# Kernel optimization log

Measured on AMD Instinct MI355X. Metric: run time of the kernel, lower is better.

Reference implementation:

```python
import jax, jax.numpy as jnp
import numpy as np

B, Q, D, H, HD, LP, M = 16, 1, 2048, 16, 128, 2048, 8192
EPS = 1e-5

def _ln(x, w, b):
    mu = jnp.mean(x, axis=-1, keepdims=True)
    var = jnp.mean((x - mu) ** 2, axis=-1, keepdims=True)
    return (x - mu) * jax.lax.rsqrt(var + EPS) * w + b

def setup_inputs() -> dict:
    key = jax.random.key(0)
    ks = jax.random.split(key, 8)
    std = 0.02
    return {
        "input": jax.random.normal(ks[0], (B, Q, D), jnp.float32),
        "past_key": jax.random.normal(ks[1], (B, LP, H, HD), jnp.float32),
        "past_value": jax.random.normal(ks[2], (B, LP, H, HD), jnp.float32),
        "ln0_w": jnp.ones((D,), jnp.float32),
        "ln0_b": jnp.zeros((D,), jnp.float32),
        "ln1_w": jnp.ones((D,), jnp.float32),
        "ln1_b": jnp.zeros((D,), jnp.float32),
        "wqkv": jax.random.normal(ks[3], (3 * D, D), jnp.float32) * std,
        "wo": jax.random.normal(ks[4], (D, D), jnp.float32) * std,
        "fc0_w": jax.random.normal(ks[5], (M, D), jnp.float32) * std,
        "fc0_b": jnp.zeros((M,), jnp.float32),
        "fc1_w": jax.random.normal(ks[6], (D, M), jnp.float32) * std,
        "fc1_b": jnp.zeros((D,), jnp.float32),
    }

def reference(input, past_key, past_value, ln0_w, ln0_b, ln1_w, ln1_b,
              wqkv, wo, fc0_w, fc0_b, fc1_w, fc1_b):
    # norm0 + fused QKV projection (no bias)
    x = _ln(input, ln0_w, ln0_b)                       # [B,Q,D]
    qkv = (x @ wqkv.T).reshape(B, Q, 3, H, HD)
    q, k, v = qkv[:, :, 0], qkv[:, :, 1], qkv[:, :, 2]  # each [B,Q,H,HD]
    # append to KV cache
    k = jnp.concatenate([past_key, k], axis=1)          # [B,LP+Q,H,HD]
    v = jnp.concatenate([past_value, v], axis=1)
    # decode attention; q_len == 1 so no causal mask is applied (matches source)
    scores = jnp.einsum('nqhd,nkhd->nhqk', q, k) / (HD ** 0.5)
    attn = jax.nn.softmax(scores.astype(jnp.float32), axis=-1).astype(scores.dtype)
    attn_out = jnp.einsum('nhql,nlhd->nqhd', attn, v).reshape(B, Q, D)
    attn_out = attn_out @ wo.T
    h = input + attn_out
    # MLP2 with exact (erf) GELU as in torch F.gelu
    y = _ln(h, ln1_w, ln1_b)
    y = jax.nn.gelu(y @ fc0_w.T + fc0_b, approximate=False) @ fc1_w.T + fc1_b
    return h + y
```

## Files before the change

kernel.cpp:

```cpp
#include <hip/hip_runtime.h>
#include <math.h>

typedef __attribute__((ext_vector_type(4))) float f32x4;
typedef __attribute__((ext_vector_type(4))) _Float16 f16x4;

#define B_  16
#define D_  2048
#define H_  16
#define HD_ 128
#define LP_ 2048
#define M_  8192
#define QKV_R (3 * D_)
#define SCALE 0.08838834764831845f
#define NSPLIT 32
#define KPS 64
#define TROWS 4
#define NT (KPS / TROWS)

__device__ inline float wave_sum(float v) {
  for (int m = 32; m > 0; m >>= 1) v += __shfl_xor(v, m);
  return v;
}

__device__ inline void gl_lds16(const float* g, float* l) {
  __builtin_amdgcn_global_load_lds(
      (const __attribute__((address_space(1))) void*)g,
      (__attribute__((address_space(3))) void*)l, 16, 0, 2 );
}

__global__ void ln_kernel(const float* __restrict__ x, const float* __restrict__ w,
                          const float* __restrict__ bb, float* __restrict__ o) {
  __shared__ float sred[4];
  int b = blockIdx.x, t = threadIdx.x;
  const float* xr = x + (size_t)b * D_;
  f32x4 v0 = *(const f32x4*)(xr + t * 8);
  f32x4 v1 = *(const f32x4*)(xr + t * 8 + 4);
  float s = (v0[0] + v0[1] + v0[2] + v0[3]) + (v1[0] + v1[1] + v1[2] + v1[3]);
  s = wave_sum(s);
  if ((t & 63) == 0) sred[t >> 6] = s;
  __syncthreads();
  float mu = (sred[0] + sred[1] + sred[2] + sred[3]) * (1.0f / D_);
  __syncthreads();
  float sq = 0.f;
  for (int i = 0; i < 4; i++) {
    float d0 = v0[i] - mu; sq += d0 * d0;
    float d1 = v1[i] - mu; sq += d1 * d1;
  }
  sq = wave_sum(sq);
  if ((t & 63) == 0) sred[t >> 6] = sq;
  __syncthreads();
  float var = (sred[0] + sred[1] + sred[2] + sred[3]) * (1.0f / D_);
  float rs = rsqrtf(var + 1e-5f);
  f32x4 w0 = *(const f32x4*)(w + t * 8), w1 = *(const f32x4*)(w + t * 8 + 4);
  f32x4 c0 = *(const f32x4*)(bb + t * 8), c1 = *(const f32x4*)(bb + t * 8 + 4);
  f32x4 o0, o1;
  for (int i = 0; i < 4; i++) {
    o0[i] = (v0[i] - mu) * rs * w0[i] + c0[i];
    o1[i] = (v1[i] - mu) * rs * w1[i] + c1[i];
  }
  *(f32x4*)(o + (size_t)b * D_ + t * 8) = o0;
  *(f32x4*)(o + (size_t)b * D_ + t * 8 + 4) = o1;
}

__global__ void gemv_k(const float* __restrict__ W, const float* __restrict__ X,
                       float* __restrict__ part, int R, int K, int kc) {
  int wave = threadIdx.x >> 6, lane = threadIdx.x & 63;
  int j0 = (blockIdx.x * 4 + wave) * 16;
  int k0 = blockIdx.y * kc;
  int col = lane & 15;
  int kg  = (lane >> 4) << 2;
  const float* wp = W + (size_t)(j0 + col) * K + k0 + kg;
  const float* xp = X + (size_t)col * K + k0 + kg;
  f32x4 acc = {0.f, 0.f, 0.f, 0.f};
  #pragma unroll 4
  for (int kk = 0; kk < kc; kk += 16) {
    f32x4 av = *(const f32x4*)xp; xp += 16;
    f32x4 bv = __builtin_nontemporal_load((const f32x4*)wp); wp += 16;
    f16x4 ah, bh;
    for (int i = 0; i < 4; i++) { ah[i] = (_Float16)av[i]; bh[i] = (_Float16)bv[i]; }
    acc = __builtin_amdgcn_mfma_f32_16x16x16f16(ah, bh, acc, 0, 0, 0);
  }
  *(f32x4*)(part + ((size_t)blockIdx.y * R + j0 + col) * 16 + kg) = acc;
}

__global__ void reduce_plain(const float* __restrict__ part, float* __restrict__ out,
                             int R, int S) {
  int i = blockIdx.x * 256 + threadIdx.x;
  int j = i >> 4, b = i & 15;
  float s = 0.f;
  for (int k = 0; k < S; k++) s += part[(size_t)k * R * 16 + i];
  out[(size_t)b * R + j] = s;
}
__global__ void reduce_resid(const float* __restrict__ part, const float* __restrict__ resid,
                             float* __restrict__ out, int R, int S) {
  int i = blockIdx.x * 256 + threadIdx.x;
  int j = i >> 4, b = i & 15;
  float s = 0.f;
  for (int k = 0; k < S; k++) s += part[(size_t)k * R * 16 + i];
  out[(size_t)b * R + j] = resid[(size_t)b * R + j] + s;
}
__global__ void reduce_bias_gelu(const float* __restrict__ part, const float* __restrict__ bias,
                                 float* __restrict__ out, int R, int S) {
  int i = blockIdx.x * 256 + threadIdx.x;
  int j = i >> 4, b = i & 15;
  float s = 0.f;
  for (int k = 0; k < S; k++) s += part[(size_t)k * R * 16 + i];
  float u = s + bias[j];
  out[(size_t)b * R + j] = 0.5f * u * (1.0f + erff(u * 0.70710678118654752f));
}
__global__ void reduce_bias_resid(const float* __restrict__ part, const float* __restrict__ bias,
                                  const float* __restrict__ resid, float* __restrict__ out,
                                  int R, int S) {
  int i = blockIdx.x * 256 + threadIdx.x;
  int j = i >> 4, b = i & 15;
  float s = 0.f;
  for (int k = 0; k < S; k++) s += part[(size_t)k * R * 16 + i];
  out[(size_t)b * R + j] = resid[(size_t)b * R + j] + s + bias[j];
}

__global__ void attn_scores(const float* __restrict__ qkv, const float* __restrict__ pk,
                            float* __restrict__ scores) {
  int b = blockIdx.x, sp = blockIdx.y;
  int t = threadIdx.x;
  int wv = __builtin_amdgcn_readfirstlane(threadIdx.x) >> 6;
  int lane = t & 63;
  int h = t >> 4, d8 = (t & 15) * 8;
  __shared__ float kbuf[2][TROWS][D_];
  __shared__ float s_t[H_][KPS + 1];

  f32x4 q0 = *(const f32x4*)(qkv + (size_t)b * QKV_R + h * HD_ + d8);
  f32x4 q1 = *(const f32x4*)(qkv + (size_t)b * QKV_R + h * HD_ + d8 + 4);
  for (int i = 0; i < 4; i++) { q0[i] *= SCALE; q1[i] *= SCALE; }

  const float* gbase = pk + ((size_t)b * LP_ + (size_t)sp * KPS) * D_;
  auto stage = [&](int buf, int tile) {
    const float* src = gbase + (size_t)tile * (TROWS * D_) + wv * 2048 + lane * 4;
    float* dst = &kbuf[buf][0][0] + wv * 2048;
    #pragma unroll
    for (int j = 0; j < 8; j++) gl_lds16(src + j * 256, dst + j * 256);
  };

  stage(0, 0);
  for (int tile = 0; tile < NT; ++tile) {
    int cur = tile & 1;
    if (tile + 1 < NT) {
      stage(cur ^ 1, tile + 1);
      __builtin_amdgcn_sched_barrier(0);
      asm volatile("s_waitcnt vmcnt(8)" ::: "memory");
    } else {
      __builtin_amdgcn_sched_barrier(0);
      asm volatile("s_waitcnt vmcnt(0)" ::: "memory");
    }
    __builtin_amdgcn_s_barrier();
    __builtin_amdgcn_sched_barrier(0);
    #pragma unroll
    for (int r = 0; r < TROWS; ++r) {
      const float* kr = &kbuf[cur][r][h * HD_ + d8];
      f32x4 k0 = *(const f32x4*)kr;
      f32x4 k1 = *(const f32x4*)(kr + 4);
      float s = q0[0]*k0[0] + q0[1]*k0[1] + q0[2]*k0[2] + q0[3]*k0[3]
              + q1[0]*k1[0] + q1[1]*k1[1] + q1[2]*k1[2] + q1[3]*k1[3];
      s += __shfl_xor(s, 1); s += __shfl_xor(s, 2);
      s += __shfl_xor(s, 4); s += __shfl_xor(s, 8);
      if ((t & 15) == 0) s_t[h][tile * TROWS + r] = s;
    }
    asm volatile("" ::: "memory");
    __builtin_amdgcn_s_barrier();
  }
  __syncthreads();
  {
    int l4 = (t & 15) * 4;
    f32x4 o;
    for (int i = 0; i < 4; i++) o[i] = s_t[h][l4 + i];
    *(f32x4*)(scores + (size_t)(b * H_ + h) * LP_ + (size_t)sp * KPS + l4) = o;
  }
}

__global__ void attn_soft(const float* __restrict__ qkv, float* __restrict__ scores,
                          float* __restrict__ pml) {
  int bh = blockIdx.x, b = bh >> 4, h = bh & 15;
  int t = threadIdx.x;
  __shared__ float sred[4];
  float prod = 0.f;
  if (t < 128) {
    float qv = qkv[(size_t)b * QKV_R + h * HD_ + t];
    float kn = qkv[(size_t)b * QKV_R + D_ + h * HD_ + t];
    prod = qv * kn;
  }
  prod = wave_sum(prod);
  if ((t & 63) == 0) sred[t >> 6] = prod;
  __syncthreads();
  float s_new = (sred[0] + sred[1] + sred[2] + sred[3]) * SCALE;
  __syncthreads();
  float* sp = scores + (size_t)bh * LP_;
  f32x4 v0 = *(const f32x4*)(sp + t * 8);
  f32x4 v1 = *(const f32x4*)(sp + t * 8 + 4);
  float m = s_new;
  for (int i = 0; i < 4; i++) m = fmaxf(m, fmaxf(v0[i], v1[i]));
  for (int mm = 32; mm > 0; mm >>= 1) m = fmaxf(m, __shfl_xor(m, mm));
  if ((t & 63) == 0) sred[t >> 6] = m;
  __syncthreads();
  float M = fmaxf(fmaxf(sred[0], sred[1]), fmaxf(sred[2], sred[3]));
  __syncthreads();
  float ls = 0.f;
  for (int i = 0; i < 4; i++) {
    v0[i] = __expf(v0[i] - M); ls += v0[i];
    v1[i] = __expf(v1[i] - M); ls += v1[i];
  }
  ls = wave_sum(ls);
  if ((t & 63) == 0) sred[t >> 6] = ls;
  __syncthreads();
  float en = __expf(s_new - M);
  float L = sred[0] + sred[1] + sred[2] + sred[3] + en;
  float inv = 1.0f / L;
  for (int i = 0; i < 4; i++) { v0[i] *= inv; v1[i] *= inv; }
  *(f32x4*)(sp + t * 8) = v0;
  *(f32x4*)(sp + t * 8 + 4) = v1;
  if (t == 0) pml[bh] = en * inv;
}

__global__ void attn_av(const float* __restrict__ scores, const float* __restrict__ pv,
                        float* __restrict__ pacc) {
  int b = blockIdx.x, sp = blockIdx.y;
  int t = threadIdx.x;
  int wv = __builtin_amdgcn_readfirstlane(threadIdx.x) >> 6;
  int lane = t & 63;
  int h = t >> 4, d8 = (t & 15) * 8;
  __shared__ float vbuf[2][TROWS][D_];
  __shared__ float p_l[H_][KPS + 1];

  {
    int l4 = (t & 15) * 4;
    f32x4 pr = *(const f32x4*)(scores + (size_t)(b * H_ + h) * LP_ + (size_t)sp * KPS + l4);
    for (int i = 0; i < 4; i++) p_l[h][l4 + i] = pr[i];
  }

  const float* gbase = pv + ((size_t)b * LP_ + (size_t)sp * KPS) * D_;
  auto stage = [&](int buf, int tile) {
    const float* src = gbase + (size_t)tile * (TROWS * D_) + wv * 2048 + lane * 4;
    float* dst = &vbuf[buf][0][0] + wv * 2048;
    #pragma unroll
    for (int j = 0; j < 8; j++) gl_lds16(src + j * 256, dst + j * 256);
  };

  stage(0, 0);
  __syncthreads();

  f32x4 a0 = {0.f, 0.f, 0.f, 0.f}, a1 = {0.f, 0.f, 0.f, 0.f};
  for (int tile = 0; tile < NT; ++tile) {
    int cur = tile & 1;
    if (tile + 1 < NT) {
      stage(cur ^ 1, tile + 1);
      __builtin_amdgcn_sched_barrier(0);
      asm volatile("s_waitcnt vmcnt(8)" ::: "memory");
    } else {
      __builtin_amdgcn_sched_barrier(0);
      asm volatile("s_waitcnt vmcnt(0)" ::: "memory");
    }
    __builtin_amdgcn_s_barrier();
    __builtin_amdgcn_sched_barrier(0);
    #pragma unroll
    for (int r = 0; r < TROWS; ++r) {
      float p = p_l[h][tile * TROWS + r];
      const float* vr = &vbuf[cur][r][h * HD_ + d8];
      f32x4 v0 = *(const f32x4*)vr;
      f32x4 v1 = *(const f32x4*)(vr + 4);
      for (int i = 0; i < 4; i++) { a0[i] += p * v0[i]; a1[i] += p * v1[i]; }
    }
    asm volatile("" ::: "memory");
    __builtin_amdgcn_s_barrier();
  }
  size_t oi = (((size_t)b * NSPLIT + sp) * H_ + h) * HD_ + d8;
  *(f32x4*)(pacc + oi) = a0;
  *(f32x4*)(pacc + oi + 4) = a1;
}

__global__ void attn_comb(const float* __restrict__ qkv, const float* __restrict__ pml,
                          const float* __restrict__ pacc, float* __restrict__ attn_out) {
  int bh = blockIdx.x, b = bh >> 4, h = bh & 15;
  int t = threadIdx.x;
  float o = 0.f;
  for (int s = 0; s < NSPLIT; s++)
    o += pacc[(((size_t)b * NSPLIT + s) * H_ + h) * HD_ + t];
  o += pml[bh] * qkv[(size_t)b * QKV_R + 2 * D_ + h * HD_ + t];
  attn_out[(size_t)b * D_ + h * HD_ + t] = o;
}

extern "C" void kernel_launch(void* const* d_in, const int* in_sizes, int n_in,
                              void* d_out, int out_size, void* d_ws, size_t ws_size,
                              hipStream_t stream) {
  const float* input  = (const float*)d_in[0];
  const float* pk     = (const float*)d_in[1];
  const float* pv     = (const float*)d_in[2];
  const float* ln0_w  = (const float*)d_in[3];
  const float* ln0_b  = (const float*)d_in[4];
  const float* ln1_w  = (const float*)d_in[5];
  const float* ln1_b  = (const float*)d_in[6];
  const float* wqkv   = (const float*)d_in[7];
  const float* wo     = (const float*)d_in[8];
  const float* fc0_w  = (const float*)d_in[9];
  const float* fc0_b  = (const float*)d_in[10];
  const float* fc1_w  = (const float*)d_in[11];
  const float* fc1_b  = (const float*)d_in[12];
  float* out = (float*)d_out;

  char* wsb = (char*)d_ws;
  float* x_ln     = (float*)(wsb + 0);
  float* qkv      = (float*)(wsb + 131072);
  float* attn_out = (float*)(wsb + 524288);
  float* hbuf     = (float*)(wsb + 655360);
  float* y0       = (float*)(wsb + 786432);
  float* act      = (float*)(wsb + 917504);
  float* scores   = (float*)(wsb + 1441792);
  float* pml      = (float*)(wsb + 3538944);
  float* pacc     = (float*)(wsb + 3543040);
  float* part     = (float*)(wsb + 11931648);

  ln_kernel<<<16, 256, 0, stream>>>(input, ln0_w, ln0_b, x_ln);
  gemv_k<<<dim3(96, 8), 256, 0, stream>>>(wqkv, x_ln, part, QKV_R, D_, 256);
  reduce_plain<<<384, 256, 0, stream>>>(part, qkv, QKV_R, 8);
  attn_scores<<<dim3(B_, NSPLIT), 256, 0, stream>>>(qkv, pk, scores);
  attn_soft<<<256, 256, 0, stream>>>(qkv, scores, pml);
  attn_av<<<dim3(B_, NSPLIT), 256, 0, stream>>>(scores, pv, pacc);
  attn_comb<<<256, 128, 0, stream>>>(qkv, pml, pacc, attn_out);
  gemv_k<<<dim3(32, 16), 256, 0, stream>>>(wo, attn_out, part, D_, D_, 128);
  reduce_resid<<<128, 256, 0, stream>>>(part, input, hbuf, D_, 16);
  ln_kernel<<<16, 256, 0, stream>>>(hbuf, ln1_w, ln1_b, y0);
  gemv_k<<<dim3(128, 4), 256, 0, stream>>>(fc0_w, y0, part, M_, D_, 512);
  reduce_bias_gelu<<<512, 256, 0, stream>>>(part, fc0_b, act, M_, 4);
  gemv_k<<<dim3(32, 16), 256, 0, stream>>>(fc1_w, act, part, D_, M_, 512);
  reduce_bias_resid<<<128, 256, 0, stream>>>(part, fc1_b, hbuf, out, D_, 16);
}
```

Baseline: 194.0 us.

## Fuse softmax into split attention with online rescale and fuse residual with LN

Removes the separate softmax kernel: each attn_av block now computes a local max and exp-sum for its KV split, and attn_comb merges the splits flash-decoding style, including the new token's score. The residual reduction and the second layernorm are merged into one kernel, which saves a launch and a round trip of hbuf. The weight loads in gemv switch from nontemporal to plain loads. The fused reduce_resid_ln runs only 16 blocks with strided part reads, so it has much less parallelism than the old reduce kernel.

```diff
diff --git a/kernel.cpp b/kernel.cpp
--- a/kernel.cpp
+++ b/kernel.cpp
@@ -75,7 +75,7 @@
   #pragma unroll 4
   for (int kk = 0; kk < kc; kk += 16) {
     f32x4 av = *(const f32x4*)xp; xp += 16;
-    f32x4 bv = __builtin_nontemporal_load((const f32x4*)wp); wp += 16;
+    f32x4 bv = *(const f32x4*)wp; wp += 16;
     f16x4 ah, bh;
     for (int i = 0; i < 4; i++) { ah[i] = (_Float16)av[i]; bh[i] = (_Float16)bv[i]; }
     acc = __builtin_amdgcn_mfma_f32_16x16x16f16(ah, bh, acc, 0, 0, 0);
@@ -90,14 +90,6 @@
   float s = 0.f;
   for (int k = 0; k < S; k++) s += part[(size_t)k * R * 16 + i];
   out[(size_t)b * R + j] = s;
-}
-__global__ void reduce_resid(const float* __restrict__ part, const float* __restrict__ resid,
-                             float* __restrict__ out, int R, int S) {
-  int i = blockIdx.x * 256 + threadIdx.x;
-  int j = i >> 4, b = i & 15;
-  float s = 0.f;
-  for (int k = 0; k < S; k++) s += part[(size_t)k * R * 16 + i];
-  out[(size_t)b * R + j] = resid[(size_t)b * R + j] + s;
 }
 __global__ void reduce_bias_gelu(const float* __restrict__ part, const float* __restrict__ bias,
                                  float* __restrict__ out, int R, int S) {
@@ -116,6 +108,42 @@
   float s = 0.f;
   for (int k = 0; k < S; k++) s += part[(size_t)k * R * 16 + i];
   out[(size_t)b * R + j] = resid[(size_t)b * R + j] + s + bias[j];
+}
+
+__global__ void reduce_resid_ln(const float* __restrict__ part, const float* __restrict__ input,
+                                const float* __restrict__ w, const float* __restrict__ bb,
+                                float* __restrict__ hbuf, float* __restrict__ y0) {
+  __shared__ float sred[4];
+  int b = blockIdx.x, t = threadIdx.x;
+  float h[8];
+  float lsum = 0.f;
+  #pragma unroll
+  for (int i = 0; i < 8; i++) {
+    int j = t + 256 * i;
+    float s = 0.f;
+    for (int k = 0; k < 16; k++) s += part[((size_t)k * D_ + j) * 16 + b];
+    h[i] = input[(size_t)b * D_ + j] + s;
+    lsum += h[i];
+  }
+  lsum = wave_sum(lsum);
+  if ((t & 63) == 0) sred[t >> 6] = lsum;
+  __syncthreads();
+  float mu = (sred[0] + sred[1] + sred[2] + sred[3]) * (1.0f / D_);
+  __syncthreads();
+  float sq = 0.f;
+  #pragma unroll
+  for (int i = 0; i < 8; i++) { float d = h[i] - mu; sq += d * d; }
+  sq = wave_sum(sq);
+  if ((t & 63) == 0) sred[t >> 6] = sq;
+  __syncthreads();
+  float var = (sred[0] + sred[1] + sred[2] + sred[3]) * (1.0f / D_);
+  float rs = rsqrtf(var + 1e-5f);
+  #pragma unroll
+  for (int i = 0; i < 8; i++) {
+    int j = t + 256 * i;
+    hbuf[(size_t)b * D_ + j] = h[i];
+    y0[(size_t)b * D_ + j] = (h[i] - mu) * rs * w[j] + bb[j];
+  }
 }
 
 __global__ void attn_scores(const float* __restrict__ qkv, const float* __restrict__ pk,
@@ -176,51 +204,8 @@
   }
 }
 
-__global__ void attn_soft(const float* __restrict__ qkv, float* __restrict__ scores,
-                          float* __restrict__ pml) {
-  int bh = blockIdx.x, b = bh >> 4, h = bh & 15;
-  int t = threadIdx.x;
-  __shared__ float sred[4];
-  float prod = 0.f;
-  if (t < 128) {
-    float qv = qkv[(size_t)b * QKV_R + h * HD_ + t];
-    float kn = qkv[(size_t)b * QKV_R + D_ + h * HD_ + t];
-    prod = qv * kn;
-  }
-  prod = wave_sum(prod);
-  if ((t & 63) == 0) sred[t >> 6] = prod;
-  __syncthreads();
-  float s_new = (sred[0] + sred[1] + sred[2] + sred[3]) * SCALE;
-  __syncthreads();
-  float* sp = scores + (size_t)bh * LP_;
-  f32x4 v0 = *(const f32x4*)(sp + t * 8);
-  f32x4 v1 = *(const f32x4*)(sp + t * 8 + 4);
-  float m = s_new;
-  for (int i = 0; i < 4; i++) m = fmaxf(m, fmaxf(v0[i], v1[i]));
-  for (int mm = 32; mm > 0; mm >>= 1) m = fmaxf(m, __shfl_xor(m, mm));
-  if ((t & 63) == 0) sred[t >> 6] = m;
-  __syncthreads();
-  float M = fmaxf(fmaxf(sred[0], sred[1]), fmaxf(sred[2], sred[3]));
-  __syncthreads();
-  float ls = 0.f;
-  for (int i = 0; i < 4; i++) {
-    v0[i] = __expf(v0[i] - M); ls += v0[i];
-    v1[i] = __expf(v1[i] - M); ls += v1[i];
-  }
-  ls = wave_sum(ls);
-  if ((t & 63) == 0) sred[t >> 6] = ls;
-  __syncthreads();
-  float en = __expf(s_new - M);
-  float L = sred[0] + sred[1] + sred[2] + sred[3] + en;
-  float inv = 1.0f / L;
-  for (int i = 0; i < 4; i++) { v0[i] *= inv; v1[i] *= inv; }
-  *(f32x4*)(sp + t * 8) = v0;
-  *(f32x4*)(sp + t * 8 + 4) = v1;
-  if (t == 0) pml[bh] = en * inv;
-}
-
 __global__ void attn_av(const float* __restrict__ scores, const float* __restrict__ pv,
-                        float* __restrict__ pacc) {
+                        float* __restrict__ pacc, float* __restrict__ pml) {
   int b = blockIdx.x, sp = blockIdx.y;
   int t = threadIdx.x;
   int wv = __builtin_amdgcn_readfirstlane(threadIdx.x) >> 6;
@@ -231,8 +216,20 @@
 
   {
     int l4 = (t & 15) * 4;
-    f32x4 pr = *(const f32x4*)(scores + (size_t)(b * H_ + h) * LP_ + (size_t)sp * KPS + l4);
-    for (int i = 0; i < 4; i++) p_l[h][l4 + i] = pr[i];
+    f32x4 sc = *(const f32x4*)(scores + (size_t)(b * H_ + h) * LP_ + (size_t)sp * KPS + l4);
+    float m = fmaxf(fmaxf(sc[0], sc[1]), fmaxf(sc[2], sc[3]));
+    m = fmaxf(m, __shfl_xor(m, 1)); m = fmaxf(m, __shfl_xor(m, 2));
+    m = fmaxf(m, __shfl_xor(m, 4)); m = fmaxf(m, __shfl_xor(m, 8));
+    f32x4 p;
+    float ls = 0.f;
+    for (int i = 0; i < 4; i++) { p[i] = __expf(sc[i] - m); ls += p[i]; }
+    ls += __shfl_xor(ls, 1); ls += __shfl_xor(ls, 2);
+    ls += __shfl_xor(ls, 4); ls += __shfl_xor(ls, 8);
+    for (int i = 0; i < 4; i++) p_l[h][l4 + i] = p[i];
+    if ((t & 15) == 0) {
+      pml[((b * NSPLIT + sp) * H_ + h) * 2]     = m;
+      pml[((b * NSPLIT + sp) * H_ + h) * 2 + 1] = ls;
+    }
   }
 
   const float* gbase = pv + ((size_t)b * LP_ + (size_t)sp * KPS) * D_;
@@ -277,13 +274,31 @@
 
 __global__ void attn_comb(const float* __restrict__ qkv, const float* __restrict__ pml,
                           const float* __restrict__ pacc, float* __restrict__ attn_out) {
-  int bh = blockIdx.x, b = bh >> 4, h = bh & 15;
+  int bh = blockIdx.x, b = bh >> 4, hh = bh & 15;
   int t = threadIdx.x;
-  float o = 0.f;
+  __shared__ float sred[2];
+  float qv = qkv[(size_t)b * QKV_R + hh * HD_ + t];
+  float kn = qkv[(size_t)b * QKV_R + D_ + hh * HD_ + t];
+  float d = qv * kn;
+  d = wave_sum(d);
+  if ((t & 63) == 0) sred[t >> 6] = d;
+  __syncthreads();
+  float s_new = (sred[0] + sred[1]) * SCALE;
+  float vn = qkv[(size_t)b * QKV_R + 2 * D_ + hh * HD_ + t];
+  float M = s_new;
   for (int s = 0; s < NSPLIT; s++)
-    o += pacc[(((size_t)b * NSPLIT + s) * H_ + h) * HD_ + t];
-  o += pml[bh] * qkv[(size_t)b * QKV_R + 2 * D_ + h * HD_ + t];
-  attn_out[(size_t)b * D_ + h * HD_ + t] = o;
+    M = fmaxf(M, pml[((b * NSPLIT + s) * H_ + hh) * 2]);
+  float en = __expf(s_new - M);
+  float L = en;
+  float o = en * vn;
+  for (int s = 0; s < NSPLIT; s++) {
+    float ms = pml[((b * NSPLIT + s) * H_ + hh) * 2];
+    float ls = pml[((b * NSPLIT + s) * H_ + hh) * 2 + 1];
+    float e = __expf(ms - M);
+    L += ls * e;
+    o += pacc[(((size_t)b * NSPLIT + s) * H_ + hh) * HD_ + t] * e;
+  }
+  attn_out[(size_t)b * D_ + hh * HD_ + t] = o / L;
 }
 
 extern "C" void kernel_launch(void* const* d_in, const int* in_sizes, int n_in,
@@ -313,19 +328,17 @@
   float* act      = (float*)(wsb + 917504);
   float* scores   = (float*)(wsb + 1441792);
   float* pml      = (float*)(wsb + 3538944);
-  float* pacc     = (float*)(wsb + 3543040);
+  float* pacc     = (float*)(wsb + 3604480);
   float* part     = (float*)(wsb + 11931648);
 
   ln_kernel<<<16, 256, 0, stream>>>(input, ln0_w, ln0_b, x_ln);
   gemv_k<<<dim3(96, 8), 256, 0, stream>>>(wqkv, x_ln, part, QKV_R, D_, 256);
   reduce_plain<<<384, 256, 0, stream>>>(part, qkv, QKV_R, 8);
   attn_scores<<<dim3(B_, NSPLIT), 256, 0, stream>>>(qkv, pk, scores);
-  attn_soft<<<256, 256, 0, stream>>>(qkv, scores, pml);
-  attn_av<<<dim3(B_, NSPLIT), 256, 0, stream>>>(scores, pv, pacc);
+  attn_av<<<dim3(B_, NSPLIT), 256, 0, stream>>>(scores, pv, pacc, pml);
   attn_comb<<<256, 128, 0, stream>>>(qkv, pml, pacc, attn_out);
   gemv_k<<<dim3(32, 16), 256, 0, stream>>>(wo, attn_out, part, D_, D_, 128);
-  reduce_resid<<<128, 256, 0, stream>>>(part, input, hbuf, D_, 16);
-  ln_kernel<<<16, 256, 0, stream>>>(hbuf, ln1_w, ln1_b, y0);
+  reduce_resid_ln<<<16, 256, 0, stream>>>(part, input, ln1_w, ln1_b, hbuf, y0);
   gemv_k<<<dim3(128, 4), 256, 0, stream>>>(fc0_w, y0, part, M_, D_, 512);
   reduce_bias_gelu<<<512, 256, 0, stream>>>(part, fc0_b, act, M_, 4);
   gemv_k<<<dim3(32, 16), 256, 0, stream>>>(fc1_w, act, part, D_, M_, 512);
```

After: 205.3 us. 5.8% more time.

## Prefetch MLP and output-projection weights into cache during attention kernels

Applied to the files above, without the earlier changes.

Adds extra blocks to the attention-score and attention-value launches. These blocks only stream fc0, fc1 and wo weight tiles through a dummy-accumulate read, so the weights sit in the last-level cache before the later GEMV kernels run. The GEMV weight loads switch from nontemporal to normal loads so they can hit those cached lines. The aim is to overlap weight fetch latency with attention work, but the prefetch competes with the streaming KV-cache reads for bandwidth and cache capacity.

```diff
diff --git a/kernel.cpp b/kernel.cpp
--- a/kernel.cpp
+++ b/kernel.cpp
@@ -16,6 +16,8 @@
 #define KPS 64
 #define TROWS 4
 #define NT (KPS / TROWS)
+#define PF_S 8
+#define PF_A 12
 
 __device__ inline float wave_sum(float v) {
   for (int m = 32; m > 0; m >>= 1) v += __shfl_xor(v, m);
@@ -26,6 +28,15 @@
   __builtin_amdgcn_global_load_lds(
       (const __attribute__((address_space(1))) void*)g,
       (__attribute__((address_space(3))) void*)l, 16, 0, 2 );
+}
+
+__device__ inline void prefetch_span(const f32x4* src, int iters, int t) {
+  f32x4 acc = {0.f, 0.f, 0.f, 0.f};
+  for (int i = 0; i < iters; i++) {
+    f32x4 v = src[(size_t)i * 256 + t];
+    for (int j = 0; j < 4; j++) acc[j] += v[j];
+  }
+  asm volatile("" :: "v"(acc[0]), "v"(acc[1]), "v"(acc[2]), "v"(acc[3]));
 }
 
 __global__ void ln_kernel(const float* __restrict__ x, const float* __restrict__ w,
@@ -75,7 +86,7 @@
   #pragma unroll 4
   for (int kk = 0; kk < kc; kk += 16) {
     f32x4 av = *(const f32x4*)xp; xp += 16;
-    f32x4 bv = __builtin_nontemporal_load((const f32x4*)wp); wp += 16;
+    f32x4 bv = *(const f32x4*)wp; wp += 16;
     f16x4 ah, bh;
     for (int i = 0; i < 4; i++) { ah[i] = (_Float16)av[i]; bh[i] = (_Float16)bv[i]; }
     acc = __builtin_amdgcn_mfma_f32_16x16x16f16(ah, bh, acc, 0, 0, 0);
@@ -119,9 +130,14 @@
 }
 
 __global__ void attn_scores(const float* __restrict__ qkv, const float* __restrict__ pk,
-                            float* __restrict__ scores) {
+                            float* __restrict__ scores, const float* __restrict__ fc0) {
   int b = blockIdx.x, sp = blockIdx.y;
   int t = threadIdx.x;
+  if (b >= B_) {
+    int pb = (b - B_) * NSPLIT + sp;
+    prefetch_span((const f32x4*)fc0 + (size_t)pb * 16384, 64, t);
+    return;
+  }
   int wv = __builtin_amdgcn_readfirstlane(threadIdx.x) >> 6;
   int lane = t & 63;
   int h = t >> 4, d8 = (t & 15) * 8;
@@ -220,9 +236,19 @@
 }
 
 __global__ void attn_av(const float* __restrict__ scores, const float* __restrict__ pv,
-                        float* __restrict__ pacc) {
+                        float* __restrict__ pacc, const float* __restrict__ fc1,
+                        const float* __restrict__ wo) {
   int b = blockIdx.x, sp = blockIdx.y;
   int t = threadIdx.x;
+  if (b >= B_) {
+    int pb = (b - B_) * NSPLIT + sp;
+    if (pb < 256) {
+      prefetch_span((const f32x4*)fc1 + (size_t)pb * 16384, 64, t);
+    } else {
+      prefetch_span((const f32x4*)wo + (size_t)(pb - 256) * 8192, 32, t);
+    }
+    return;
+  }
   int wv = __builtin_amdgcn_readfirstlane(threadIdx.x) >> 6;
   int lane = t & 63;
   int h = t >> 4, d8 = (t & 15) * 8;
@@ -319,9 +345,9 @@
   ln_kernel<<<16, 256, 0, stream>>>(input, ln0_w, ln0_b, x_ln);
   gemv_k<<<dim3(96, 8), 256, 0, stream>>>(wqkv, x_ln, part, QKV_R, D_, 256);
   reduce_plain<<<384, 256, 0, stream>>>(part, qkv, QKV_R, 8);
-  attn_scores<<<dim3(B_, NSPLIT), 256, 0, stream>>>(qkv, pk, scores);
+  attn_scores<<<dim3(B_ + PF_S, NSPLIT), 256, 0, stream>>>(qkv, pk, scores, fc0_w);
   attn_soft<<<256, 256, 0, stream>>>(qkv, scores, pml);
-  attn_av<<<dim3(B_, NSPLIT), 256, 0, stream>>>(scores, pv, pacc);
+  attn_av<<<dim3(B_ + PF_A, NSPLIT), 256, 0, stream>>>(scores, pv, pacc, fc1_w, wo);
   attn_comb<<<256, 128, 0, stream>>>(qkv, pml, pacc, attn_out);
   gemv_k<<<dim3(32, 16), 256, 0, stream>>>(wo, attn_out, part, D_, D_, 128);
   reduce_resid<<<128, 256, 0, stream>>>(part, input, hbuf, D_, 16);
```

Result: slower. 218.4 us (+12.6%).
